# Kernel optimization log

Hardware: AMD Instinct MI355X
Metric: run time of the kernel (lower is better)

Reference implementation:

```python
import jax, jax.numpy as jnp
import numpy as np

B, T, D_MODEL, HEAD_DIM = 4, 4096, 1024, 2


def setup_inputs() -> dict:
    key = jax.random.key(0)
    kx, kq, kk, kv = jax.random.split(key, 4)
    x = jax.random.normal(kx, (B, T, D_MODEL), dtype=jnp.float32)
    # nn.Linear weights: (out_features, in_features), applied as x @ W.T
    s_qk = 1.0 / np.sqrt(D_MODEL)
    W_Q = jax.random.uniform(kq, (HEAD_DIM, D_MODEL), minval=-s_qk, maxval=s_qk, dtype=jnp.float32)
    W_K = jax.random.uniform(kk, (HEAD_DIM, D_MODEL), minval=-s_qk, maxval=s_qk, dtype=jnp.float32)
    W_V = jax.random.uniform(kv, (D_MODEL, D_MODEL), minval=-s_qk, maxval=s_qk, dtype=jnp.float32)
    # strict upper-triangular True = masked (future positions)
    causal_mask = jnp.triu(jnp.ones((T, T), dtype=bool), k=1)[None, :, :]
    return {"x": x, "W_Q": W_Q, "W_K": W_K, "W_V": W_V, "causal_mask": causal_mask}


def reference(x, W_Q, W_K, W_V, causal_mask):
    # x: (B, T, d_model)
    Q = jnp.einsum('btd,hd->bth', x, W_Q)   # (B, T, head_dim)
    K = jnp.einsum('bsd,hd->bsh', x, W_K)   # (B, S, head_dim)
    V = jnp.einsum('bsd,ed->bse', x, W_V)   # (B, S, d_model)
    scores = jnp.einsum('bth,bsh->bts', Q, K)              # (B, T, S)
    scores = jnp.where(causal_mask, -jnp.inf, scores)
    max_idx = jnp.argmax(scores, axis=-1)                  # (B, T)
    # one-hot scatter + bmm in the original == hard gather of V rows
    out = jnp.take_along_axis(V, max_idx[..., None], axis=1)  # (B, T, d_model)
    return out
```

## Files before the change

kernel.cpp:

```cpp
#include <hip/hip_runtime.h>
#include <math.h>

#define TT 4096
#define DM 1024
#define BB 4
#define BT (BB * TT)
#define SENTINEL 0x7fffffff


__device__ __forceinline__ float dot4(const float4 a, const float4 b) {
    return a.x * b.x + a.y * b.y + a.z * b.z + a.w * b.w;
}

__global__ __launch_bounds__(256) void qk_kernel(const float* __restrict__ x,
                                                 const float* __restrict__ wq,
                                                 const float* __restrict__ wk,
                                                 float* __restrict__ Q,
                                                 float* __restrict__ K,
                                                 int* __restrict__ rep,
                                                 int* __restrict__ cnt) {
    const int tid = threadIdx.x;
    const int wave = tid >> 6, lane = tid & 63;
    const int row0 = blockIdx.x * 8;

    if (tid < 8) rep[row0 + tid] = SENTINEL;
    if (row0 == 0 && tid == 8) cnt[0] = 0;

    float4 wq0[4], wq1[4], wk0[4], wk1[4];
    #pragma unroll
    for (int j = 0; j < 4; ++j) {
        wq0[j] = ((const float4*)(wq))[j * 64 + lane];
        wq1[j] = ((const float4*)(wq + DM))[j * 64 + lane];
        wk0[j] = ((const float4*)(wk))[j * 64 + lane];
        wk1[j] = ((const float4*)(wk + DM))[j * 64 + lane];
    }
    #pragma unroll
    for (int i = 0; i < 2; ++i) {
        const int row = row0 + i * 4 + wave;
        const float4* xr = (const float4*)(x + (size_t)row * DM);
        float s0 = 0.f, s1 = 0.f, s2 = 0.f, s3 = 0.f;
        #pragma unroll
        for (int j = 0; j < 4; ++j) {
            const float4 xv = xr[j * 64 + lane];
            s0 += dot4(xv, wq0[j]);
            s1 += dot4(xv, wq1[j]);
            s2 += dot4(xv, wk0[j]);
            s3 += dot4(xv, wk1[j]);
        }
        #pragma unroll
        for (int off = 32; off > 0; off >>= 1) {
            s0 += __shfl_down(s0, off);
            s1 += __shfl_down(s1, off);
            s2 += __shfl_down(s2, off);
            s3 += __shfl_down(s3, off);
        }
        if (lane == 0) {
            ((float2*)Q)[row] = make_float2(s0, s1);
            ((float2*)K)[row] = make_float2(s2, s3);
        }
    }
}

__global__ __launch_bounds__(256) void argmax_kernel(const float* __restrict__ Q,
                                                     const float* __restrict__ K,
                                                     int* __restrict__ idx,
                                                     int* __restrict__ rep,
                                                     int* __restrict__ list,
                                                     int* __restrict__ vpos,
                                                     int* __restrict__ cnt) {
    __shared__ float2 ks[TT];
    const int b   = blockIdx.x >> 10;
    const int tgr = blockIdx.x & 1023;
    const int tg  = ((tgr & 31) << 5) | (tgr >> 5);
    const int tid = threadIdx.x;
    const int nfill = tg * 4 + 4;

    const float2* kb = (const float2*)(K + (size_t)b * TT * 2);
    for (int i = tid; i < nfill; i += 256) ks[i] = kb[i];
    __syncthreads();

    const int wave = tid >> 6, lane = tid & 63;
    const int t = tg * 4 + wave;
    const float2 q = ((const float2*)Q)[b * TT + t];
    const float4* kp = (const float4*)ks;

    float best = -INFINITY;
    int bi = 0x7fffffff;
    int p = lane;
    while (2 * (p + 64) + 1 <= t) {
        const float4 a = kp[p];
        const float4 c = kp[p + 64];
        const float c0 = q.x * a.x + q.y * a.y;
        const float c1 = q.x * a.z + q.y * a.w;
        const float c2 = q.x * c.x + q.y * c.y;
        const float c3 = q.x * c.z + q.y * c.w;
        if (c0 > best) { best = c0; bi = 2 * p; }
        if (c1 > best) { best = c1; bi = 2 * p + 1; }
        if (c2 > best) { best = c2; bi = 2 * (p + 64); }
        if (c3 > best) { best = c3; bi = 2 * (p + 64) + 1; }
        p += 128;
    }
    while (2 * p <= t) {
        const float4 a = kp[p];
        const float c0 = q.x * a.x + q.y * a.y;
        if (c0 > best) { best = c0; bi = 2 * p; }
        if (2 * p + 1 <= t) {
            const float c1 = q.x * a.z + q.y * a.w;
            if (c1 > best) { best = c1; bi = 2 * p + 1; }
        }
        p += 64;
    }
    #pragma unroll
    for (int off = 32; off > 0; off >>= 1) {
        const float ov = __shfl_down(best, off);
        const int   oi = __shfl_down(bi, off);
        if (ov > best || (ov == best && oi < bi)) { best = ov; bi = oi; }
    }
    if (lane == 0) {
        idx[b * TT + t] = bi;
        const int bs = b * TT + bi;
        const int old = atomicMin(&rep[bs], t);
        if (old == SENTINEL) {
            const int pp = atomicAdd(cnt, 1);
            list[pp] = bs;
            vpos[bs] = pp;
        }
    }
}

__global__ __launch_bounds__(256) void vrow_kernel(const float* __restrict__ x,
                                                   const float* __restrict__ wv,
                                                   const int* __restrict__ list,
                                                   const int* __restrict__ cnt,
                                                   float* __restrict__ vrows) {
    const int tid = threadIdx.x, wave = tid >> 6, lane = tid & 63;
    const int slice = blockIdx.x >> 4;
    const int usub  = blockIdx.x & 15;
    const int e0 = slice * 16 + wave * 4;

    float4 w[4][4];
    #pragma unroll
    for (int r = 0; r < 4; ++r) {
        const float4* wr = (const float4*)(wv + (size_t)(e0 + r) * DM);
        #pragma unroll
        for (int j = 0; j < 4; ++j) w[r][j] = wr[j * 64 + lane];
    }

    const int n = cnt[0];
    for (int li = usub; li < n; li += 16) {
        const int bs = list[li];
        const float4* xr = (const float4*)(x + (size_t)bs * DM);
        float4 xv[4];
        #pragma unroll
        for (int j = 0; j < 4; ++j) xv[j] = xr[j * 64 + lane];

        float s0 = 0.f, s1 = 0.f, s2 = 0.f, s3 = 0.f;
        #pragma unroll
        for (int j = 0; j < 4; ++j) {
            s0 += dot4(w[0][j], xv[j]);
            s1 += dot4(w[1][j], xv[j]);
            s2 += dot4(w[2][j], xv[j]);
            s3 += dot4(w[3][j], xv[j]);
        }
        #pragma unroll
        for (int off = 32; off > 0; off >>= 1) {
            s0 += __shfl_down(s0, off);
            s1 += __shfl_down(s1, off);
            s2 += __shfl_down(s2, off);
            s3 += __shfl_down(s3, off);
        }
        if (lane == 0)
            *(float4*)(vrows + (size_t)li * DM + e0) = make_float4(s0, s1, s2, s3);
    }
}

__global__ __launch_bounds__(256) void gather_kernel(const int* __restrict__ idx,
                                                     const int* __restrict__ vpos,
                                                     const float* __restrict__ vrows,
                                                     float* __restrict__ out) {
    __shared__ int sli[16];
    const int tid = threadIdx.x;
    const int row0 = blockIdx.x * 16;
    if (tid < 16) {
        const int bt = row0 + tid;
        const int b = bt >> 12;
        sli[tid] = vpos[b * TT + idx[bt]];
    }
    __syncthreads();
    #pragma unroll 4
    for (int i = 0; i < 16; ++i) {
        const float4* src = (const float4*)(vrows + (size_t)sli[i] * DM);
        float4* dst = (float4*)(out + (size_t)(row0 + i) * DM);
        dst[tid] = src[tid];
    }
}

extern "C" void kernel_launch(void* const* d_in, const int* in_sizes, int n_in,
                              void* d_out, int out_size, void* d_ws, size_t ws_size,
                              hipStream_t stream) {
    const float* x  = (const float*)d_in[0];
    const float* wq = (const float*)d_in[1];
    const float* wk = (const float*)d_in[2];
    const float* wv = (const float*)d_in[3];
    float* out = (float*)d_out;

    char* ws = (char*)d_ws;
    float* Q     = (float*)(ws);
    float* K     = (float*)(ws + 131072);
    int*   idx   = (int*)  (ws + 262144);
    int*   rep   = (int*)  (ws + 327680);
    int*   list  = (int*)  (ws + 393216);
    int*   vpos  = (int*)  (ws + 458752);
    int*   cnt   = (int*)  (ws + 524288);
    float* vrows = (float*)(ws + 1048576);

    qk_kernel<<<BT / 8, 256, 0, stream>>>(x, wq, wk, Q, K, rep, cnt);
    argmax_kernel<<<4096, 256, 0, stream>>>(Q, K, idx, rep, list, vpos, cnt);
    vrow_kernel<<<1024, 256, 0, stream>>>(x, wv, list, cnt, vrows);
    gather_kernel<<<BT / 16, 256, 0, stream>>>(idx, vpos, vrows, out);
}
```

Baseline: 222.2 us.

## Shrink rows per block in QK and gather kernels, early-exit idle vrow blocks

```diff
diff --git a/kernel.cpp b/kernel.cpp
--- a/kernel.cpp
+++ b/kernel.cpp
@@ -21,10 +21,10 @@
                                                  int* __restrict__ cnt) {
     const int tid = threadIdx.x;
     const int wave = tid >> 6, lane = tid & 63;
-    const int row0 = blockIdx.x * 8;
-
-    if (tid < 8) rep[row0 + tid] = SENTINEL;
-    if (row0 == 0 && tid == 8) cnt[0] = 0;
+    const int row0 = blockIdx.x * 4;
+
+    if (tid < 4) rep[row0 + tid] = SENTINEL;
+    if (row0 == 0 && tid == 4) cnt[0] = 0;
 
     float4 wq0[4], wq1[4], wk0[4], wk1[4];
     #pragma unroll
@@ -34,30 +34,30 @@
         wk0[j] = ((const float4*)(wk))[j * 64 + lane];
         wk1[j] = ((const float4*)(wk + DM))[j * 64 + lane];
     }
-    #pragma unroll
-    for (int i = 0; i < 2; ++i) {
-        const int row = row0 + i * 4 + wave;
-        const float4* xr = (const float4*)(x + (size_t)row * DM);
-        float s0 = 0.f, s1 = 0.f, s2 = 0.f, s3 = 0.f;
-        #pragma unroll
-        for (int j = 0; j < 4; ++j) {
-            const float4 xv = xr[j * 64 + lane];
-            s0 += dot4(xv, wq0[j]);
-            s1 += dot4(xv, wq1[j]);
-            s2 += dot4(xv, wk0[j]);
-            s3 += dot4(xv, wk1[j]);
-        }
-        #pragma unroll
-        for (int off = 32; off > 0; off >>= 1) {
-            s0 += __shfl_down(s0, off);
-            s1 += __shfl_down(s1, off);
-            s2 += __shfl_down(s2, off);
-            s3 += __shfl_down(s3, off);
-        }
-        if (lane == 0) {
-            ((float2*)Q)[row] = make_float2(s0, s1);
-            ((float2*)K)[row] = make_float2(s2, s3);
-        }
+    const int row = row0 + wave;
+    const float4* xr = (const float4*)(x + (size_t)row * DM);
+    float4 xv[4];
+    #pragma unroll
+    for (int j = 0; j < 4; ++j) xv[j] = xr[j * 64 + lane];
+
+    float s0 = 0.f, s1 = 0.f, s2 = 0.f, s3 = 0.f;
+    #pragma unroll
+    for (int j = 0; j < 4; ++j) {
+        s0 += dot4(xv[j], wq0[j]);
+        s1 += dot4(xv[j], wq1[j]);
+        s2 += dot4(xv[j], wk0[j]);
+        s3 += dot4(xv[j], wk1[j]);
+    }
+    #pragma unroll
+    for (int off = 32; off > 0; off >>= 1) {
+        s0 += __shfl_down(s0, off);
+        s1 += __shfl_down(s1, off);
+        s2 += __shfl_down(s2, off);
+        s3 += __shfl_down(s3, off);
+    }
+    if (lane == 0) {
+        ((float2*)Q)[row] = make_float2(s0, s1);
+        ((float2*)K)[row] = make_float2(s2, s3);
     }
 }
 
@@ -68,28 +68,27 @@
                                                      int* __restrict__ list,
                                                      int* __restrict__ vpos,
                                                      int* __restrict__ cnt) {
-    __shared__ float2 ks[TT];
+    __shared__ float4 ks4[TT / 2];
     const int b   = blockIdx.x >> 10;
     const int tgr = blockIdx.x & 1023;
     const int tg  = ((tgr & 31) << 5) | (tgr >> 5);
     const int tid = threadIdx.x;
-    const int nfill = tg * 4 + 4;
-
-    const float2* kb = (const float2*)(K + (size_t)b * TT * 2);
-    for (int i = tid; i < nfill; i += 256) ks[i] = kb[i];
+    const int nfill4 = tg * 2 + 2;
+
+    const float4* kb4 = (const float4*)(K + (size_t)b * TT * 2);
+    for (int i = tid; i < nfill4; i += 256) ks4[i] = kb4[i];
     __syncthreads();
 
     const int wave = tid >> 6, lane = tid & 63;
     const int t = tg * 4 + wave;
     const float2 q = ((const float2*)Q)[b * TT + t];
-    const float4* kp = (const float4*)ks;
 
     float best = -INFINITY;
     int bi = 0x7fffffff;
     int p = lane;
     while (2 * (p + 64) + 1 <= t) {
-        const float4 a = kp[p];
-        const float4 c = kp[p + 64];
+        const float4 a = ks4[p];
+        const float4 c = ks4[p + 64];
         const float c0 = q.x * a.x + q.y * a.y;
         const float c1 = q.x * a.z + q.y * a.w;
         const float c2 = q.x * c.x + q.y * c.y;
@@ -101,7 +100,7 @@
         p += 128;
     }
     while (2 * p <= t) {
-        const float4 a = kp[p];
+        const float4 a = ks4[p];
         const float c0 = q.x * a.x + q.y * a.y;
         if (c0 > best) { best = c0; bi = 2 * p; }
         if (2 * p + 1 <= t) {
@@ -119,8 +118,7 @@
     if (lane == 0) {
         idx[b * TT + t] = bi;
         const int bs = b * TT + bi;
-        const int old = atomicMin(&rep[bs], t);
-        if (old == SENTINEL) {
+        if (atomicMin(&rep[bs], t) == SENTINEL) {
             const int pp = atomicAdd(cnt, 1);
             list[pp] = bs;
             vpos[bs] = pp;
@@ -136,8 +134,10 @@
     const int tid = threadIdx.x, wave = tid >> 6, lane = tid & 63;
     const int slice = blockIdx.x >> 4;
     const int usub  = blockIdx.x & 15;
+    const int n = cnt[0];
+    if (usub >= n) return;
+
     const int e0 = slice * 16 + wave * 4;
-
     float4 w[4][4];
     #pragma unroll
     for (int r = 0; r < 4; ++r) {
@@ -146,7 +146,6 @@
         for (int j = 0; j < 4; ++j) w[r][j] = wr[j * 64 + lane];
     }
 
-    const int n = cnt[0];
     for (int li = usub; li < n; li += 16) {
         const int bs = list[li];
         const float4* xr = (const float4*)(x + (size_t)bs * DM);
@@ -178,21 +177,23 @@
                                                      const int* __restrict__ vpos,
                                                      const float* __restrict__ vrows,
                                                      float* __restrict__ out) {
-    __shared__ int sli[16];
+    __shared__ int sli[4];
     const int tid = threadIdx.x;
-    const int row0 = blockIdx.x * 16;
-    if (tid < 16) {
+    const int row0 = blockIdx.x * 4;
+    if (tid < 4) {
         const int bt = row0 + tid;
         const int b = bt >> 12;
         sli[tid] = vpos[b * TT + idx[bt]];
     }
     __syncthreads();
-    #pragma unroll 4
-    for (int i = 0; i < 16; ++i) {
-        const float4* src = (const float4*)(vrows + (size_t)sli[i] * DM);
-        float4* dst = (float4*)(out + (size_t)(row0 + i) * DM);
-        dst[tid] = src[tid];
-    }
+    const float4 v0 = ((const float4*)(vrows + (size_t)sli[0] * DM))[tid];
+    const float4 v1 = ((const float4*)(vrows + (size_t)sli[1] * DM))[tid];
+    const float4 v2 = ((const float4*)(vrows + (size_t)sli[2] * DM))[tid];
+    const float4 v3 = ((const float4*)(vrows + (size_t)sli[3] * DM))[tid];
+    ((float4*)(out + (size_t)(row0 + 0) * DM))[tid] = v0;
+    ((float4*)(out + (size_t)(row0 + 1) * DM))[tid] = v1;
+    ((float4*)(out + (size_t)(row0 + 2) * DM))[tid] = v2;
+    ((float4*)(out + (size_t)(row0 + 3) * DM))[tid] = v3;
 }
 
 extern "C" void kernel_launch(void* const* d_in, const int* in_sizes, int n_in,
@@ -214,8 +215,8 @@
     int*   cnt   = (int*)  (ws + 524288);
     float* vrows = (float*)(ws + 1048576);
 
-    qk_kernel<<<BT / 8, 256, 0, stream>>>(x, wq, wk, Q, K, rep, cnt);
+    qk_kernel<<<BT / 4, 256, 0, stream>>>(x, wq, wk, Q, K, rep, cnt);
     argmax_kernel<<<4096, 256, 0, stream>>>(Q, K, idx, rep, list, vpos, cnt);
     vrow_kernel<<<1024, 256, 0, stream>>>(x, wv, list, cnt, vrows);
-    gather_kernel<<<BT / 16, 256, 0, stream>>>(idx, vpos, vrows, out);
-}
+    gather_kernel<<<BT / 4, 256, 0, stream>>>(idx, vpos, vrows, out);
+}
```

Result: faster. 217.5 us (-2.1%).
